# Kernel optimization log

Hardware: AMD Instinct MI355X
Metric: run time of the kernel (lower is better)

Reference implementation:

```python
import jax, jax.numpy as jnp
import numpy as np

X, Y, DIM = 256, 256, 512
N = X * Y
NUM_ITERS = 100
LEARNING_RADIUS = 0.3
COGNITIVE = 0.1
SOCIAL = 0.1
INERTIA = 0.5
SIGMA = max(X, Y) / 2.0  # source default: sigma = max(x, y) / 2.0


def setup_inputs() -> dict:
    key = jax.random.key(0)
    k1, k2, k3, k4 = jax.random.split(key, 4)
    gx, gy = jnp.meshgrid(jnp.arange(X), jnp.arange(Y), indexing='ij')
    grid_locations = jnp.stack([gx.ravel(), gy.ravel()], axis=1).astype(jnp.int32)  # [N,2]
    return {
        "input": jax.random.normal(k1, (DIM,), dtype=jnp.float32),
        "particles": jax.random.normal(k2, (N, DIM), dtype=jnp.float32),
        "velocities": jnp.zeros((N, DIM), dtype=jnp.float32),
        "r1": jax.random.uniform(k3, (N, DIM), dtype=jnp.float32),
        "r2": jax.random.uniform(k4, (N, DIM), dtype=jnp.float32),
        "grid_locations": grid_locations,
        "iter_num": 10,
    }


def reference(input, particles, velocities, r1, r2, grid_locations, iter_num):
    # BMU: pairwise L2 distance of input against all particles, argmin.
    diff_in = input[None, :] - particles                      # [N, D]
    dists = jnp.sqrt(jnp.sum(diff_in * diff_in, axis=1))      # [N]
    bmu_idx = jnp.argmin(dists)

    # Decayed learning radius / sigma.
    decay = 1.0 - iter_num / NUM_ITERS
    radius = LEARNING_RADIUS * decay
    sigma_d = SIGMA * decay

    # Gaussian neighborhood over the 2D grid around the BMU location.
    bmu_loc = grid_locations[bmu_idx].astype(jnp.float32)     # [2]
    d2 = jnp.sum((grid_locations.astype(jnp.float32) - bmu_loc[None, :]) ** 2, axis=1)  # [N]
    neighborhood = jnp.exp(-d2 / (sigma_d ** 2))              # [N]

    # PSO update (vectorized form of the per-particle/per-dim loop).
    global_best = particles[bmu_idx]                          # [D]
    global_nbest = neighborhood[bmu_idx]                      # scalar (== 1.0)
    update_mask = (global_nbest - neighborhood) <= radius     # [N]; skipped particles keep state

    diff = global_best[None, :] - particles                   # [N, D]
    v_new = INERTIA * velocities + COGNITIVE * r1 * diff + SOCIAL * r2 * diff
    # NOTE: the clamp of p_update to [0,1] in the source is dead code; the
    # particle is assigned particle + v_update unconditionally.
    m = update_mask[:, None]
    new_velocities = jnp.where(m, v_new, velocities)
    new_particles = jnp.where(m, particles + v_new, particles)
    return new_particles, new_velocities
```

## Files before the change

kernel.cpp:

```cpp
#include <hip/hip_runtime.h>


constexpr int DIM   = 512;
constexpr int NPART = 256 * 256;
constexpr int THREADS = 256;
constexpr int WPB = THREADS / 64;
constexpr int DIST_BLOCKS = 2048;

__global__ __launch_bounds__(THREADS)
void som_dist(const float* __restrict__ input,
              const float* __restrict__ particles,
              unsigned long long* __restrict__ partials) {
    const int lane = threadIdx.x & 63;
    const int wave = threadIdx.x >> 6;
    const int gwave  = blockIdx.x * WPB + wave;
    const int nwaves = gridDim.x * WPB;

    const float4* in4 = (const float4*)input;
    const float4 i0 = in4[lane];
    const float4 i1 = in4[64 + lane];

    unsigned long long best = ~0ull;
    for (int row = gwave; row < NPART; row += nwaves) {
        const float4* p4 = (const float4*)(particles + (size_t)row * DIM);
        float4 p0 = p4[lane];
        float4 p1 = p4[64 + lane];
        float t, d;
        t = i0.x - p0.x; d  = t * t;
        t = i0.y - p0.y; d += t * t;
        t = i0.z - p0.z; d += t * t;
        t = i0.w - p0.w; d += t * t;
        t = i1.x - p1.x; d += t * t;
        t = i1.y - p1.y; d += t * t;
        t = i1.z - p1.z; d += t * t;
        t = i1.w - p1.w; d += t * t;
        #pragma unroll
        for (int off = 32; off >= 1; off >>= 1)
            d += __shfl_xor(d, off, 64);
        unsigned long long enc =
            ((unsigned long long)__float_as_uint(d) << 32) | (unsigned int)row;
        best = (enc < best) ? enc : best;
    }

    __shared__ unsigned long long smin[WPB];
    if (lane == 0) smin[wave] = best;
    __syncthreads();
    if (threadIdx.x == 0) {
        unsigned long long b = smin[0];
        #pragma unroll
        for (int i = 1; i < WPB; ++i) b = (smin[i] < b) ? smin[i] : b;
        partials[blockIdx.x] = b;
    }
}

__global__ __launch_bounds__(256)
void som_reduce(const unsigned long long* __restrict__ partials,
                unsigned long long* __restrict__ out) {
    __shared__ unsigned long long s[256];
    unsigned long long b = ~0ull;
    for (int i = threadIdx.x; i < DIST_BLOCKS; i += 256) {
        unsigned long long v = partials[i];
        b = (v < b) ? v : b;
    }
    s[threadIdx.x] = b;
    __syncthreads();
    for (int off = 128; off >= 1; off >>= 1) {
        if (threadIdx.x < off) {
            unsigned long long v = s[threadIdx.x + off];
            if (v < s[threadIdx.x]) s[threadIdx.x] = v;
        }
        __syncthreads();
    }
    if (threadIdx.x == 0) out[0] = s[0];
}

__global__ __launch_bounds__(THREADS)
void som_update(const float* __restrict__ particles,
                const float* __restrict__ velocities,
                const float* __restrict__ r1,
                const float* __restrict__ r2,
                const int*   __restrict__ grid_loc,
                const int*   __restrict__ iter_num,
                const unsigned long long* __restrict__ bmu_enc,
                float* __restrict__ out_p,
                float* __restrict__ out_v) {
    const int lane = threadIdx.x & 63;
    const int wave = threadIdx.x >> 6;
    const int row  = blockIdx.x * WPB + wave;

    const int bmu = (int)(unsigned int)(bmu_enc[0] & 0xffffffffull);
    const float decay   = 1.0f - (float)iter_num[0] * (1.0f / 100.0f);
    const float radius  = 0.3f * decay;
    const float sigma_d = 128.0f * decay;

    const int2 gl = ((const int2*)grid_loc)[row];
    const int2 bl = ((const int2*)grid_loc)[bmu];
    const float dx = (float)gl.x - (float)bl.x;
    const float dy = (float)gl.y - (float)bl.y;
    const float d2 = dx * dx + dy * dy;
    const float nb = expf(-d2 / (sigma_d * sigma_d));
    const bool upd = (1.0f - nb) <= radius;

    const size_t base = (size_t)row * DIM;
    const float4* p4 = (const float4*)(particles  + base);
    const float4* v4 = (const float4*)(velocities + base);
    float4* op4 = (float4*)(out_p + base);
    float4* ov4 = (float4*)(out_v + base);

    if (!upd) {
        float4 a0 = p4[lane], a1 = p4[64 + lane];
        float4 b0 = v4[lane], b1 = v4[64 + lane];
        op4[lane] = a0; op4[64 + lane] = a1;
        ov4[lane] = b0; ov4[64 + lane] = b1;
    } else {
        const float4* g4 = (const float4*)(particles + (size_t)bmu * DIM);
        const float4* x4 = (const float4*)(r1 + base);
        const float4* y4 = (const float4*)(r2 + base);
        #pragma unroll
        for (int h = 0; h < 2; ++h) {
            const int idx = h * 64 + lane;
            float4 p = p4[idx], v = v4[idx], g = g4[idx];
            float4 a = x4[idx], b = y4[idx];
            float4 vn, po;
            float df;
            df = g.x - p.x; vn.x = 0.5f * v.x + 0.1f * a.x * df + 0.1f * b.x * df;
            df = g.y - p.y; vn.y = 0.5f * v.y + 0.1f * a.y * df + 0.1f * b.y * df;
            df = g.z - p.z; vn.z = 0.5f * v.z + 0.1f * a.z * df + 0.1f * b.z * df;
            df = g.w - p.w; vn.w = 0.5f * v.w + 0.1f * a.w * df + 0.1f * b.w * df;
            po.x = p.x + vn.x; po.y = p.y + vn.y;
            po.z = p.z + vn.z; po.w = p.w + vn.w;
            ov4[idx] = vn;
            op4[idx] = po;
        }
    }
}

extern "C" void kernel_launch(void* const* d_in, const int* in_sizes, int n_in,
                              void* d_out, int out_size, void* d_ws, size_t ws_size,
                              hipStream_t stream) {
    const float* input      = (const float*)d_in[0];
    const float* particles  = (const float*)d_in[1];
    const float* velocities = (const float*)d_in[2];
    const float* r1         = (const float*)d_in[3];
    const float* r2         = (const float*)d_in[4];
    const int*   grid_loc   = (const int*)d_in[5];
    const int*   iter_num   = (const int*)d_in[6];

    float* out_p = (float*)d_out;
    float* out_v = out_p + (size_t)NPART * DIM;

    unsigned long long* w        = (unsigned long long*)d_ws;
    unsigned long long* final_enc = w;
    unsigned long long* partials  = w + 8;

    som_dist<<<DIST_BLOCKS, THREADS, 0, stream>>>(input, particles, partials);
    som_reduce<<<1, 256, 0, stream>>>(partials, final_enc);
    som_update<<<NPART / WPB, THREADS, 0, stream>>>(
        particles, velocities, r1, r2, grid_loc, iter_num, final_enc,
        out_p, out_v);
}
```

Measured before the change: 130.1 us.

## Fuse distance, argmin reduction and PSO update into one cooperative kernel

Result: slower. 375.4 us (+188.5%).

```diff
diff --git a/kernel.cpp b/kernel.cpp
--- a/kernel.cpp
+++ b/kernel.cpp
@@ -1,136 +1,153 @@
 #include <hip/hip_runtime.h>
+#include <hip/hip_cooperative_groups.h>
+
+namespace cg = cooperative_groups;
 
 
-constexpr int DIM   = 512;
-constexpr int NPART = 256 * 256;
+typedef float v4f __attribute__((ext_vector_type(4)));
+
+constexpr int DIM     = 512;
+constexpr int NPART   = 256 * 256;
 constexpr int THREADS = 256;
-constexpr int WPB = THREADS / 64;
-constexpr int DIST_BLOCKS = 2048;
+constexpr int WPB     = THREADS / 64;
+constexpr int BLOCKS  = 1024;
+constexpr int NWAVES  = BLOCKS * WPB;
+constexpr int RPW     = NPART / NWAVES;
 
-__global__ __launch_bounds__(THREADS)
-void som_dist(const float* __restrict__ input,
-              const float* __restrict__ particles,
-              unsigned long long* __restrict__ partials) {
-    const int lane = threadIdx.x & 63;
-    const int wave = threadIdx.x >> 6;
-    const int gwave  = blockIdx.x * WPB + wave;
-    const int nwaves = gridDim.x * WPB;
+__global__ __launch_bounds__(THREADS, 4)
+void som_fused(const float* __restrict__ input,
+               const float* __restrict__ particles,
+               const float* __restrict__ velocities,
+               const float* __restrict__ r1,
+               const float* __restrict__ r2,
+               const int*   __restrict__ grid_loc,
+               const int*   __restrict__ iter_num,
+               unsigned long long* __restrict__ partials,
+               float* __restrict__ out_p,
+               float* __restrict__ out_v) {
+    const int lane  = threadIdx.x & 63;
+    const int wave  = threadIdx.x >> 6;
+    const int gwave = blockIdx.x * WPB + wave;
 
-    const float4* in4 = (const float4*)input;
-    const float4 i0 = in4[lane];
-    const float4 i1 = in4[64 + lane];
+    __shared__ unsigned long long sred[THREADS];
+
+    const v4f* in4 = (const v4f*)input;
+    const v4f i0 = in4[lane];
+    const v4f i1 = in4[64 + lane];
 
     unsigned long long best = ~0ull;
-    for (int row = gwave; row < NPART; row += nwaves) {
-        const float4* p4 = (const float4*)(particles + (size_t)row * DIM);
-        float4 p0 = p4[lane];
-        float4 p1 = p4[64 + lane];
-        float t, d;
-        t = i0.x - p0.x; d  = t * t;
-        t = i0.y - p0.y; d += t * t;
-        t = i0.z - p0.z; d += t * t;
-        t = i0.w - p0.w; d += t * t;
-        t = i1.x - p1.x; d += t * t;
-        t = i1.y - p1.y; d += t * t;
-        t = i1.z - p1.z; d += t * t;
-        t = i1.w - p1.w; d += t * t;
+    for (int i = 0; i < RPW; i += 2) {
+        const int rowA = gwave + i * NWAVES;
+        const int rowB = rowA + NWAVES;
+        const v4f* pa = (const v4f*)(particles + (size_t)rowA * DIM);
+        const v4f* pb = (const v4f*)(particles + (size_t)rowB * DIM);
+        v4f a0 = pa[lane], a1 = pa[64 + lane];
+        v4f b0 = pb[lane], b1 = pb[64 + lane];
+
+        v4f t, accA, accB;
+        t = i0 - a0; accA  = t * t;
+        t = i1 - a1; accA += t * t;
+        t = i0 - b0; accB  = t * t;
+        t = i1 - b1; accB += t * t;
+        float dA = accA.x + accA.y + accA.z + accA.w;
+        float dB = accB.x + accB.y + accB.z + accB.w;
         #pragma unroll
-        for (int off = 32; off >= 1; off >>= 1)
-            d += __shfl_xor(d, off, 64);
-        unsigned long long enc =
-            ((unsigned long long)__float_as_uint(d) << 32) | (unsigned int)row;
-        best = (enc < best) ? enc : best;
+        for (int off = 32; off >= 1; off >>= 1) {
+            dA += __shfl_xor(dA, off, 64);
+            dB += __shfl_xor(dB, off, 64);
+        }
+        unsigned long long encA =
+            ((unsigned long long)__float_as_uint(dA) << 32) | (unsigned int)rowA;
+        unsigned long long encB =
+            ((unsigned long long)__float_as_uint(dB) << 32) | (unsigned int)rowB;
+        best = (encA < best) ? encA : best;
+        best = (encB < best) ? encB : best;
     }
 
-    __shared__ unsigned long long smin[WPB];
-    if (lane == 0) smin[wave] = best;
+    if (lane == 0) sred[wave] = best;
     __syncthreads();
     if (threadIdx.x == 0) {
-        unsigned long long b = smin[0];
+        unsigned long long b = sred[0];
         #pragma unroll
-        for (int i = 1; i < WPB; ++i) b = (smin[i] < b) ? smin[i] : b;
-        partials[blockIdx.x] = b;
+        for (int i = 1; i < WPB; ++i) b = (sred[i] < b) ? sred[i] : b;
+        __hip_atomic_store(&partials[blockIdx.x], b,
+                           __ATOMIC_RELEASE, __HIP_MEMORY_SCOPE_AGENT);
     }
-}
 
-__global__ __launch_bounds__(256)
-void som_reduce(const unsigned long long* __restrict__ partials,
-                unsigned long long* __restrict__ out) {
-    __shared__ unsigned long long s[256];
+    cg::this_grid().sync();
+
     unsigned long long b = ~0ull;
-    for (int i = threadIdx.x; i < DIST_BLOCKS; i += 256) {
-        unsigned long long v = partials[i];
+    for (int i = threadIdx.x; i < BLOCKS; i += THREADS) {
+        unsigned long long v = __hip_atomic_load(&partials[i],
+                                __ATOMIC_ACQUIRE, __HIP_MEMORY_SCOPE_AGENT);
         b = (v < b) ? v : b;
     }
-    s[threadIdx.x] = b;
+    sred[threadIdx.x] = b;
     __syncthreads();
+    #pragma unroll
     for (int off = 128; off >= 1; off >>= 1) {
         if (threadIdx.x < off) {
-            unsigned long long v = s[threadIdx.x + off];
-            if (v < s[threadIdx.x]) s[threadIdx.x] = v;
+            unsigned long long v = sred[threadIdx.x + off];
+            if (v < sred[threadIdx.x]) sred[threadIdx.x] = v;
         }
         __syncthreads();
     }
-    if (threadIdx.x == 0) out[0] = s[0];
-}
+    const unsigned long long enc = sred[0];
+    const int bmu = (int)(unsigned int)(enc & 0xffffffffull);
 
-__global__ __launch_bounds__(THREADS)
-void som_update(const float* __restrict__ particles,
-                const float* __restrict__ velocities,
-                const float* __restrict__ r1,
-                const float* __restrict__ r2,
-                const int*   __restrict__ grid_loc,
-                const int*   __restrict__ iter_num,
-                const unsigned long long* __restrict__ bmu_enc,
-                float* __restrict__ out_p,
-                float* __restrict__ out_v) {
-    const int lane = threadIdx.x & 63;
-    const int wave = threadIdx.x >> 6;
-    const int row  = blockIdx.x * WPB + wave;
-
-    const int bmu = (int)(unsigned int)(bmu_enc[0] & 0xffffffffull);
     const float decay   = 1.0f - (float)iter_num[0] * (1.0f / 100.0f);
     const float radius  = 0.3f * decay;
     const float sigma_d = 128.0f * decay;
+    const float s2      = sigma_d * sigma_d;
 
-    const int2 gl = ((const int2*)grid_loc)[row];
-    const int2 bl = ((const int2*)grid_loc)[bmu];
-    const float dx = (float)gl.x - (float)bl.x;
-    const float dy = (float)gl.y - (float)bl.y;
-    const float d2 = dx * dx + dy * dy;
-    const float nb = expf(-d2 / (sigma_d * sigma_d));
-    const bool upd = (1.0f - nb) <= radius;
+    const int2* gl2 = (const int2*)grid_loc;
+    const int2 bl = gl2[bmu];
+    const float blx = (float)bl.x, bly = (float)bl.y;
 
-    const size_t base = (size_t)row * DIM;
-    const float4* p4 = (const float4*)(particles  + base);
-    const float4* v4 = (const float4*)(velocities + base);
-    float4* op4 = (float4*)(out_p + base);
-    float4* ov4 = (float4*)(out_v + base);
+    const v4f* g4 = (const v4f*)(particles + (size_t)bmu * DIM);
+    const v4f g0 = g4[lane];
+    const v4f g1 = g4[64 + lane];
 
-    if (!upd) {
-        float4 a0 = p4[lane], a1 = p4[64 + lane];
-        float4 b0 = v4[lane], b1 = v4[64 + lane];
-        op4[lane] = a0; op4[64 + lane] = a1;
-        ov4[lane] = b0; ov4[64 + lane] = b1;
-    } else {
-        const float4* g4 = (const float4*)(particles + (size_t)bmu * DIM);
-        const float4* x4 = (const float4*)(r1 + base);
-        const float4* y4 = (const float4*)(r2 + base);
-        #pragma unroll
-        for (int h = 0; h < 2; ++h) {
-            const int idx = h * 64 + lane;
-            float4 p = p4[idx], v = v4[idx], g = g4[idx];
-            float4 a = x4[idx], b = y4[idx];
-            float4 vn, po;
-            float df;
-            df = g.x - p.x; vn.x = 0.5f * v.x + 0.1f * a.x * df + 0.1f * b.x * df;
-            df = g.y - p.y; vn.y = 0.5f * v.y + 0.1f * a.y * df + 0.1f * b.y * df;
-            df = g.z - p.z; vn.z = 0.5f * v.z + 0.1f * a.z * df + 0.1f * b.z * df;
-            df = g.w - p.w; vn.w = 0.5f * v.w + 0.1f * a.w * df + 0.1f * b.w * df;
-            po.x = p.x + vn.x; po.y = p.y + vn.y;
-            po.z = p.z + vn.z; po.w = p.w + vn.w;
-            ov4[idx] = vn;
-            op4[idx] = po;
+    for (int i = 0; i < RPW; ++i) {
+        const int row = (NPART - 1) - (gwave + i * NWAVES);
+        const int2 gl = gl2[row];
+        const float dx = (float)gl.x - blx;
+        const float dy = (float)gl.y - bly;
+        const float d2 = dx * dx + dy * dy;
+        const float nb = expf(-d2 / s2);
+        const bool upd = (1.0f - nb) <= radius;
+
+        const size_t base = (size_t)row * DIM;
+        const v4f* p4  = (const v4f*)(particles  + base);
+        const v4f* vv4 = (const v4f*)(velocities + base);
+        v4f* op4 = (v4f*)(out_p + base);
+        v4f* ov4 = (v4f*)(out_v + base);
+
+        if (!upd) {
+            v4f a0 = p4[lane], a1 = p4[64 + lane];
+            v4f c0 = __builtin_nontemporal_load(vv4 + lane);
+            v4f c1 = __builtin_nontemporal_load(vv4 + 64 + lane);
+            __builtin_nontemporal_store(a0, op4 + lane);
+            __builtin_nontemporal_store(a1, op4 + 64 + lane);
+            __builtin_nontemporal_store(c0, ov4 + lane);
+            __builtin_nontemporal_store(c1, ov4 + 64 + lane);
+        } else {
+            const v4f* x4 = (const v4f*)(r1 + base);
+            const v4f* y4 = (const v4f*)(r2 + base);
+            #pragma unroll
+            for (int h = 0; h < 2; ++h) {
+                const int idx = h * 64 + lane;
+                v4f p = p4[idx];
+                v4f v = __builtin_nontemporal_load(vv4 + idx);
+                v4f a = __builtin_nontemporal_load(x4 + idx);
+                v4f c = __builtin_nontemporal_load(y4 + idx);
+                v4f g = h ? g1 : g0;
+                v4f df = g - p;
+                v4f vn = 0.5f * v + 0.1f * a * df + 0.1f * c * df;
+                v4f po = p + vn;
+                __builtin_nontemporal_store(vn, ov4 + idx);
+                __builtin_nontemporal_store(po, op4 + idx);
+            }
         }
     }
 }
@@ -149,13 +166,14 @@
     float* out_p = (float*)d_out;
     float* out_v = out_p + (size_t)NPART * DIM;
 
-    unsigned long long* w        = (unsigned long long*)d_ws;
-    unsigned long long* final_enc = w;
-    unsigned long long* partials  = w + 8;
+    unsigned long long* partials = (unsigned long long*)d_ws;
 
-    som_dist<<<DIST_BLOCKS, THREADS, 0, stream>>>(input, particles, partials);
-    som_reduce<<<1, 256, 0, stream>>>(partials, final_enc);
-    som_update<<<NPART / WPB, THREADS, 0, stream>>>(
-        particles, velocities, r1, r2, grid_loc, iter_num, final_enc,
-        out_p, out_v);
+    void* args[] = {
+        (void*)&input, (void*)&particles, (void*)&velocities,
+        (void*)&r1, (void*)&r2, (void*)&grid_loc, (void*)&iter_num,
+        (void*)&partials, (void*)&out_p, (void*)&out_v
+    };
+    hipLaunchCooperativeKernel((const void*)som_fused,
+                               dim3(BLOCKS), dim3(THREADS),
+                               args, 0, stream);
 }
```
